# Optimization experiments

Measured on AMD Instinct MI355X. Metric: run time of the kernel, lower is better.

## Reference

```python
import jax, jax.numpy as jnp
import numpy as np

B, S, C, HEADS = 1, 4096, 640, 8
AH, AW = 64, 64            # attn-resolution grid, AH*AW == S
MH, MW = 512, 512          # full-res mask size
NEG = -1e9                 # finite large negative (safe for fully-masked rows)


def nearest_resize(x, h, w):
    # torch F.interpolate(mode='nearest'): idx = floor(i * H_in / H_out)
    H, W = x.shape[-2], x.shape[-1]
    ri = (jnp.arange(h) * H) // h
    ci = (jnp.arange(w) * W) // w
    return x[..., ri, :][..., :, ci]


def sdpa(q, k, v, mask, heads):
    # q,k,v: [B,S,C]; mask: [B,1,S,S] bool (True = attend), broadcasts over heads
    b, s, c = q.shape
    d = c // heads
    qh = q.reshape(b, s, heads, d).transpose(0, 2, 1, 3)  # bhsd
    kh = k.reshape(b, s, heads, d).transpose(0, 2, 1, 3)
    vh = v.reshape(b, s, heads, d).transpose(0, 2, 1, 3)
    scores = jnp.einsum('bhqd,bhkd->bhqk', qh, kh) / jnp.sqrt(jnp.asarray(d, qh.dtype))
    scores = jnp.where(mask, scores, NEG)
    attn = jax.nn.softmax(scores, axis=-1)
    out = jnp.einsum('bhqk,bhkd->bhqd', attn, vh)
    return out.transpose(0, 2, 1, 3).reshape(b, s, c)


def setup_inputs():
    key = jax.random.key(0)
    ks = jax.random.split(key, 14)
    std = 1.0 / np.sqrt(C)
    w = lambda k: (jax.random.normal(k, (C, C), jnp.float32) * std)
    return {
        'hidden_states': jax.random.normal(ks[0], (B, S, C), jnp.float32),
        'mask': jax.random.randint(ks[1], (B, 1, MH, MW), 0, 4, jnp.int32),
        'inpainting_mask': jax.random.randint(ks[2], (B, 1, MH, MW), 0, 2, jnp.int32),
        'Wq': w(ks[3]), 'Wk': w(ks[4]), 'Wv': w(ks[5]),
        'Wq_ent': w(ks[6]), 'Wk_ent': w(ks[7]), 'Wv_ent': w(ks[8]),
        'Wq_out': w(ks[9]), 'Wk_out': w(ks[10]), 'Wv_out': w(ks[11]),
        'Wo': w(ks[12]),
    }


def reference(hidden_states, mask, inpainting_mask, Wq, Wk, Wv,
              Wq_ent, Wk_ent, Wv_ent, Wq_out, Wk_out, Wv_out, Wo):
    residual = hidden_states
    b, s, c = hidden_states.shape

    # --- interpolation-derived masks (kept as [B,1,S,S]; broadcasts over heads) ---
    m = nearest_resize(mask, AH, AW).reshape(b, 1, s)                 # entity labels
    attn_mask = m[:, :, :, None] == m[:, :, None, :]                  # same-entity [B,1,S,S]
    im = nearest_resize(inpainting_mask, AH, AW).reshape(b, 1, s)
    outside_key = (im[:, :, None, :] == 0)                            # [B,1,1,S]
    attn_mask_outside = attn_mask & outside_key                       # [B,1,S,S]

    # --- projections ---
    q = hidden_states @ Wq.T
    k = hidden_states @ Wk.T
    v = hidden_states @ Wv.T
    q_e = hidden_states @ Wq_ent.T
    k_e = hidden_states @ Wk_ent.T
    v_e = hidden_states @ Wv_ent.T
    q_o = hidden_states @ Wq_out.T
    k_o = hidden_states @ Wk_out.T
    v_o = hidden_states @ Wv_out.T

    # --- three SDPA branches ---
    hs_orig = sdpa(q, k, v, attn_mask, HEADS)            # original attention
    hs_ent = sdpa(q_e, k_e, v_e, attn_mask, 1)           # entity attention (1 head)
    hs_out = sdpa(q_o, k_o, v_o, attn_mask_outside, HEADS)  # outside attention

    hs = hs_orig + hs_ent + hs_out
    return hs @ Wo.T + residual
```

## Files before the change

### kernel.cpp

```cpp
#include <hip/hip_runtime.h>
#include <cstdint>

typedef __attribute__((ext_vector_type(8))) short bf16x8;
typedef __attribute__((ext_vector_type(4))) short bf16x4;
typedef __attribute__((ext_vector_type(4))) float f32x4;

#define S_LEN 4096
#define CDIM  640
#define NPROJ 5760

__device__ __forceinline__ f32x4 mfma16(bf16x4 a, bf16x4 b, f32x4 c){
#if defined(__HIP_DEVICE_COMPILE__) && __HIP_DEVICE_COMPILE__
  return __builtin_amdgcn_mfma_f32_16x16x16bf16_1k(a, b, c, 0, 0, 0);
#else
  (void)a; (void)b;
  return c;
#endif
}

__device__ __forceinline__ void gload_lds(const unsigned short* g, unsigned short* l){
#if defined(__HIP_DEVICE_COMPILE__) && __HIP_DEVICE_COMPILE__
  __builtin_amdgcn_global_load_lds((const __attribute__((address_space(1))) unsigned int*)g,
                                   (__attribute__((address_space(3))) unsigned int*)l, 16, 0, 0);
#else
  (void)g; (void)l;
#endif
}

__device__ __forceinline__ unsigned short f2bf(float f){
  union { float f; uint32_t u; } v; v.f = f;
  uint32_t u = v.u;
  return (unsigned short)((u + 0x7fffu + ((u >> 16) & 1u)) >> 16);
}
__device__ __forceinline__ float b2f(unsigned short h){
  union { uint32_t u; float f; } v; v.u = ((uint32_t)h) << 16;
  return v.f;
}

__global__ void k_labels(const int* __restrict__ mask, const int* __restrict__ inp,
                         int* __restrict__ labels){
  int s = blockIdx.x * 256 + threadIdx.x;
  if (s >= S_LEN) return;
  int y = s >> 6, x = s & 63;
  int off = (y * 8) * 512 + x * 8;
  int m = mask[off] & 0xff;
  int o = (inp[off] == 0) ? 0x100 : 0;
  labels[s] = m | o;
}

__global__ void k_hist(const int* __restrict__ labels, int* __restrict__ boff, int* __restrict__ cnt){
  __shared__ int h[4];
  if (threadIdx.x < 4) h[threadIdx.x] = 0;
  __syncthreads();
  for (int s = threadIdx.x; s < S_LEN; s += 256) atomicAdd(&h[labels[s] & 3], 1);
  __syncthreads();
  if (threadIdx.x == 0){
    int a = 0;
    for (int c = 0; c < 4; c++){ boff[c] = a; a += h[c]; }
    boff[4] = a;
  }
  if (threadIdx.x < 4) cnt[threadIdx.x] = 0;
}

__global__ void k_perm(const int* __restrict__ labels, const int* __restrict__ boff,
                       int* __restrict__ cnt, int* __restrict__ perm,
                       int* __restrict__ inv, int* __restrict__ labP){
  int s = blockIdx.x * 256 + threadIdx.x;
  if (s >= S_LEN) return;
  int lab = labels[s];
  int c = lab & 3;
  int pos = boff[c] + atomicAdd(&cnt[c], 1);
  perm[pos] = s; inv[s] = pos; labP[pos] = lab;
}

__global__ void k_tiles(const int* __restrict__ labP, const int* __restrict__ boff,
                        int4* __restrict__ qtinfo, float* __restrict__ rowsum){
  int t = threadIdx.x;
  __shared__ int nkt[32];
  if (t < 32){
    int c0 = labP[t * 128] & 3, c1 = labP[t * 128 + 127] & 3;
    int lo = boff[c0] & ~127, hi = (boff[c1 + 1] + 127) & ~127;
    qtinfo[t].x = lo; qtinfo[t].y = hi; qtinfo[t].w = 0;
    nkt[t] = (hi - lo) >> 7;
  }
  __syncthreads();
  if (t == 0){
    int a = 0;
    for (int i = 0; i < 32; i++){ qtinfo[i].z = a; a += nkt[i]; }
  }
  for (int s = t; s < S_LEN; s += 256) rowsum[s] = 0.f;
}

__global__ void k_cvt_hs(const float* __restrict__ src, unsigned short* __restrict__ dst, int n){
  int idx = (blockIdx.x * 256 + threadIdx.x) * 4;
  if (idx >= n) return;
  float4 v = *(const float4*)(src + idx);
  ushort4 o;
  o.x = f2bf(v.x); o.y = f2bf(v.y); o.z = f2bf(v.z); o.w = f2bf(v.w);
  *(ushort4*)(dst + idx) = o;
}

struct WPtrs { const float* w[10]; };

__global__ void k_cvt_w(WPtrs p, unsigned short* __restrict__ dst){
  int e = (blockIdx.x * 256 + threadIdx.x) * 4;
  if (e >= 10 * 409600) return;
  int a = e / 409600, r = e % 409600;
  float sc = (a == 0 || a == 6) ? 0.11180339887498948f
           : (a == 3 ? 0.03952847075210474f : 1.0f);
  float4 v = *(const float4*)(p.w[a] + r);
  ushort4 o;
  o.x = f2bf(v.x * sc); o.y = f2bf(v.y * sc); o.z = f2bf(v.z * sc); o.w = f2bf(v.w * sc);
  *(ushort4*)(dst + e) = o;
}

template<int EPI>
__global__ __launch_bounds__(256) void k_gemm(const unsigned short* __restrict__ A,
                                              const unsigned short* __restrict__ B,
                                              int M, int N, int K, int ldc,
                                              const int* __restrict__ rowmap,
                                              unsigned short* __restrict__ Cb,
                                              float* __restrict__ Cf,
                                              const float* __restrict__ resid){
  __shared__ __align__(16) unsigned short As[128 * 64];
  __shared__ __align__(16) unsigned short Bs[128 * 64];
  int m0 = blockIdx.y * 128, n0 = blockIdx.x * 128;
  int tid = threadIdx.x;
  int wid = tid >> 6, lane = tid & 63;
  int quad = lane >> 4, l16 = lane & 15;
  int wm = (wid >> 1) * 64, wn = (wid & 1) * 64;
  f32x4 acc[4][4];
#pragma unroll
  for (int i = 0; i < 4; i++)
#pragma unroll
    for (int j = 0; j < 4; j++) acc[i][j] = f32x4{0.f, 0.f, 0.f, 0.f};

  for (int k0 = 0; k0 < K; k0 += 64){
    __syncthreads();
#pragma unroll
    for (int u = 0; u < 4; u++){
      int c = tid + u * 256;
      int row = c >> 3, off = (c & 7) * 8;
      gload_lds(&A[(size_t)(m0 + row) * K + k0 + off], &As[c * 8]);
      gload_lds(&B[(size_t)(n0 + row) * K + k0 + off], &Bs[c * 8]);
    }
    __syncthreads();
#pragma unroll
    for (int ks = 0; ks < 2; ks++){
      bf16x8 af[4], bfr[4];
#pragma unroll
      for (int t = 0; t < 4; t++){
        af[t]  = *(const bf16x8*)(&As[(wm + t * 16 + l16) * 64 + ks * 32 + quad * 8]);
        bfr[t] = *(const bf16x8*)(&Bs[(wn + t * 16 + l16) * 64 + ks * 32 + quad * 8]);
      }
#pragma unroll
      for (int mt = 0; mt < 4; mt++)
#pragma unroll
        for (int nt = 0; nt < 4; nt++)
          acc[mt][nt] = __builtin_amdgcn_mfma_f32_16x16x32_bf16(af[mt], bfr[nt], acc[mt][nt], 0, 0, 0);
    }
  }
#pragma unroll
  for (int mt = 0; mt < 4; mt++)
#pragma unroll
    for (int nt = 0; nt < 4; nt++)
#pragma unroll
      for (int r = 0; r < 4; r++){
        int row = m0 + wm + mt * 16 + quad * 4 + r;
        int col = n0 + wn + nt * 16 + l16;
        float v = acc[mt][nt][r];
        if (EPI == 0){
          Cb[(size_t)rowmap[row] * ldc + col] = f2bf(v);
        } else {
          int ro = rowmap[row];
          Cf[(size_t)ro * ldc + col] = v + resid[(size_t)ro * ldc + col];
        }
      }
}

__global__ void k_transpose_v(const unsigned short* __restrict__ proj, unsigned short* __restrict__ vT){
  __shared__ unsigned short T[64][65];
  int z = blockIdx.z;
  int s0 = blockIdx.x * 64, c0 = blockIdx.y * 64;
  int colbase = 1280 + z * 1920 + c0;
  unsigned short* dst = vT + (size_t)z * CDIM * S_LEN;
  int tid = threadIdx.x;
  for (int i = tid; i < 64 * 64; i += 256){
    int r = i >> 6, c = i & 63;
    T[r][c] = proj[(size_t)(s0 + r) * NPROJ + colbase + c];
  }
  __syncthreads();
  for (int i = tid; i < 64 * 64; i += 256){
    int c = i >> 6, r = i & 63;
    dst[(size_t)(c0 + c) * S_LEN + s0 + r] = T[r][c];
  }
}

#define KP 84
#define VP 76
__global__ __launch_bounds__(512, 2) void k_attn80(const unsigned short* __restrict__ proj,
                                                   const unsigned short* __restrict__ vT,
                                                   const int* __restrict__ labP,
                                                   const int4* __restrict__ qtinfo,
                                                   unsigned short* __restrict__ opart,
                                                   float* __restrict__ lpP){
  __shared__ __align__(16) unsigned short Ks[2][64 * KP];
  __shared__ __align__(16) unsigned short Vt[2][80 * VP];
  __shared__ __align__(16) int labk[2][64];
  int tid = threadIdx.x, wid = tid >> 6, lane = tid & 63;
  int quad = lane >> 4, l16 = lane & 15;
  int qt = blockIdx.x >> 1, half = blockIdx.x & 1;
  int q0 = qt * 256;
  int h  = blockIdx.y;
  bool OUTSIDE = (blockIdx.z == 1);
  int qc = (OUTSIDE ? 3840 : 0) + h * 80;
  int kc = (OUTSIDE ? 4480 : 640) + h * 80;
  const unsigned short* vTb = vT + (size_t)(OUTSIDE ? 2 : 0) * CDIM * S_LEN;
  int4 qa = qtinfo[qt * 2], qb = qtinfo[qt * 2 + 1];
  int lo = min(qa.x, qb.x), hi = max(qa.y, qb.y);
  int t0 = lo >> 6, t1 = hi >> 6;
  int nt = t1 - t0;
  int mid = t0 + ((nt + 1) >> 1);
  int ta = half ? mid : t0;
  int tb = half ? t1 : mid;

  int qrow0 = q0 + wid * 32 + l16;
  int qrow1 = qrow0 + 16;
  bf16x4 qf0[5], qf1[5];
#pragma unroll
  for (int dc = 0; dc < 5; dc++){
    qf0[dc] = *(const bf16x4*)&proj[(size_t)qrow0 * NPROJ + qc + dc * 16 + quad * 4];
    qf1[dc] = *(const bf16x4*)&proj[(size_t)qrow1 * NPROJ + qc + dc * 16 + quad * 4];
  }
  int lq0 = labP[qrow0] & 0xff, lq1 = labP[qrow1] & 0xff;

  float lp0 = 0.f, lp1 = 0.f;
  f32x4 Oc0[5], Oc1[5];
#pragma unroll
  for (int t = 0; t < 5; t++){ Oc0[t] = f32x4{0.f,0.f,0.f,0.f}; Oc1[t] = f32x4{0.f,0.f,0.f,0.f}; }

  const bool ISK = (tid < 256);
  const int t5 = ISK ? tid : (tid - 256);
  const unsigned short* gb = ISK ? proj : vTb;
  const int km = ISK ? NPROJ : 1;
  int ga0, ga1, ga2, ga3, ga4, ls0, ls1, ls2, ls3, ls4;
  {
    const int c0_ = t5, c1_ = t5 + 256, c2_ = t5 + 512, c3_ = t5 + 768, c4_ = t5 + 1024;
    if (ISK){
      ga0 = (c0_ / 20) * NPROJ + kc + (c0_ % 20) * 4;
      ga1 = (c1_ / 20) * NPROJ + kc + (c1_ % 20) * 4;
      ga2 = (c2_ / 20) * NPROJ + kc + (c2_ % 20) * 4;
      ga3 = (c3_ / 20) * NPROJ + kc + (c3_ % 20) * 4;
      ga4 = (c4_ / 20) * NPROJ + kc + (c4_ % 20) * 4;
      ls0 = (c0_ / 20) * KP + (c0_ % 20) * 4;
      ls1 = (c1_ / 20) * KP + (c1_ % 20) * 4;
      ls2 = (c2_ / 20) * KP + (c2_ % 20) * 4;
      ls3 = (c3_ / 20) * KP + (c3_ % 20) * 4;
      ls4 = (c4_ / 20) * KP + (c4_ % 20) * 4;
    } else {
      ga0 = (h * 80 + (c0_ >> 4)) * S_LEN + (c0_ & 15) * 4;
      ga1 = (h * 80 + (c1_ >> 4)) * S_LEN + (c1_ & 15) * 4;
      ga2 = (h * 80 + (c2_ >> 4)) * S_LEN + (c2_ & 15) * 4;
      ga3 = (h * 80 + (c3_ >> 4)) * S_LEN + (c3_ & 15) * 4;
      ga4 = (h * 80 + (c4_ >> 4)) * S_LEN + (c4_ & 15) * 4;
      ls0 = (c0_ >> 4) * VP + (c0_ & 15) * 4;
      ls1 = (c1_ >> 4) * VP + (c1_ & 15) * 4;
      ls2 = (c2_ >> 4) * VP + (c2_ & 15) * 4;
      ls3 = (c3_ >> 4) * VP + (c3_ & 15) * 4;
      ls4 = (c4_ >> 4) * VP + (c4_ & 15) * 4;
    }
  }

  uint2 r0, r1, r2, r3, r4;
  int lreg = 0;

#define LOADT(kt_) do {                                              \
    size_t _ob = (size_t)((kt_) * 64) * (size_t)km;                  \
    r0 = *(const uint2*)&gb[_ob + ga0];                              \
    r1 = *(const uint2*)&gb[_ob + ga1];                              \
    r2 = *(const uint2*)&gb[_ob + ga2];                              \
    r3 = *(const uint2*)&gb[_ob + ga3];                              \
    r4 = *(const uint2*)&gb[_ob + ga4];                              \
    if (tid < 64) lreg = labP[(kt_) * 64 + tid];                     \
  } while (0)

#define WRITET(b) do {                                               \
    unsigned short* _lb = ISK ? Ks[b] : Vt[b];                       \
    *(uint2*)&_lb[ls0] = r0;                                         \
    *(uint2*)&_lb[ls1] = r1;                                         \
    *(uint2*)&_lb[ls2] = r2;                                         \
    *(uint2*)&_lb[ls3] = r3;                                         \
    *(uint2*)&_lb[ls4] = r4;                                         \
    if (tid < 64) labk[b][tid] = lreg;                               \
  } while (0)

  LOADT(ta);
  WRITET(0);
  if (ta + 1 < tb) LOADT(ta + 1);
  __syncthreads();

  int cur = 0;
  for (int kt = ta; kt < tb; kt++){
    int nxt = cur ^ 1;
    if (kt + 1 < tb){
      WRITET(nxt);
      if (kt + 2 < tb) LOADT(kt + 2);
    }

#pragma unroll
    for (int kg = 0; kg < 4; kg++){
      f32x4 sa0 = f32x4{0.f,0.f,0.f,0.f}, sa1 = f32x4{0.f,0.f,0.f,0.f};
#pragma unroll
      for (int dc = 0; dc < 5; dc++){
        bf16x4 kf = *(const bf16x4*)&Ks[cur][(kg * 16 + l16) * KP + dc * 16 + quad * 4];
        sa0 = mfma16(kf, qf0[dc], sa0);
        sa1 = mfma16(kf, qf1[dc], sa1);
      }
      int4 lk4 = *(const int4*)&labk[cur][kg * 16 + quad * 4];
      bool m0 = !OUTSIDE || (lk4.x & 0x100), m1 = !OUTSIDE || (lk4.y & 0x100);
      bool m2 = !OUTSIDE || (lk4.z & 0x100), m3 = !OUTSIDE || (lk4.w & 0x100);
      int k0l = lk4.x & 0xff, k1l = lk4.y & 0xff, k2l = lk4.z & 0xff, k3l = lk4.w & 0xff;
      bf16x4 pf0, pf1;
      {
        float p0 = (k0l == lq0 && m0) ? __expf(sa0[0]) : 0.f;
        float p1 = (k1l == lq0 && m1) ? __expf(sa0[1]) : 0.f;
        float p2 = (k2l == lq0 && m2) ? __expf(sa0[2]) : 0.f;
        float p3 = (k3l == lq0 && m3) ? __expf(sa0[3]) : 0.f;
        lp0 += (p0 + p1) + (p2 + p3);
        pf0[0] = (short)f2bf(p0); pf0[1] = (short)f2bf(p1);
        pf0[2] = (short)f2bf(p2); pf0[3] = (short)f2bf(p3);
      }
      {
        float p0 = (k0l == lq1 && m0) ? __expf(sa1[0]) : 0.f;
        float p1 = (k1l == lq1 && m1) ? __expf(sa1[1]) : 0.f;
        float p2 = (k2l == lq1 && m2) ? __expf(sa1[2]) : 0.f;
        float p3 = (k3l == lq1 && m3) ? __expf(sa1[3]) : 0.f;
        lp1 += (p0 + p1) + (p2 + p3);
        pf1[0] = (short)f2bf(p0); pf1[1] = (short)f2bf(p1);
        pf1[2] = (short)f2bf(p2); pf1[3] = (short)f2bf(p3);
      }
#pragma unroll
      for (int dt = 0; dt < 5; dt++){
        bf16x4 vf = *(const bf16x4*)&Vt[cur][(dt * 16 + l16) * VP + kg * 16 + quad * 4];
        Oc0[dt] = mfma16(vf, pf0, Oc0[dt]);
        Oc1[dt] = mfma16(vf, pf1, Oc1[dt]);
      }
    }
    __syncthreads();
    cur = nxt;
  }
#undef LOADT
#undef WRITET
  lp0 += __shfl_xor(lp0, 16); lp0 += __shfl_xor(lp0, 32);
  lp1 += __shfl_xor(lp1, 16); lp1 += __shfl_xor(lp1, 32);
  int hz = half * 2 + (int)blockIdx.z;
  if (quad == 0){
    lpP[(size_t)(hz * 8 + h) * S_LEN + qrow0] = lp0;
    lpP[(size_t)(hz * 8 + h) * S_LEN + qrow1] = lp1;
  }
  unsigned short* dst = opart + (size_t)hz * S_LEN * CDIM;
#pragma unroll
  for (int dt = 0; dt < 5; dt++){
    ushort4 o;
    o.x = f2bf(Oc0[dt][0]); o.y = f2bf(Oc0[dt][1]);
    o.z = f2bf(Oc0[dt][2]); o.w = f2bf(Oc0[dt][3]);
    *(ushort4*)&dst[(size_t)qrow0 * CDIM + h * 80 + dt * 16 + quad * 4] = o;
    o.x = f2bf(Oc1[dt][0]); o.y = f2bf(Oc1[dt][1]);
    o.z = f2bf(Oc1[dt][2]); o.w = f2bf(Oc1[dt][3]);
    *(ushort4*)&dst[(size_t)qrow1 * CDIM + h * 80 + dt * 16 + quad * 4] = o;
  }
}

__global__ __launch_bounds__(256) void k_comb(const unsigned short* __restrict__ opart,
                                              const float* __restrict__ lpP,
                                              unsigned short* __restrict__ planes){
  int i = blockIdx.x * 256 + threadIdx.x;
  int z = blockIdx.y;
  int qrow = i / 160, c4 = (i % 160) * 4;
  int h = c4 / 80;
  size_t o0 = ((size_t)(z)     * S_LEN + qrow) * CDIM + c4;
  size_t o1 = ((size_t)(2 + z) * S_LEN + qrow) * CDIM + c4;
  float lp = lpP[(size_t)(z * 8 + h) * S_LEN + qrow]
           + lpP[(size_t)((2 + z) * 8 + h) * S_LEN + qrow];
  float iL = 1.f / lp;
  ushort4 a = *(const ushort4*)&opart[o0];
  ushort4 b = *(const ushort4*)&opart[o1];
  ushort4 o;
  o.x = f2bf((b2f(a.x) + b2f(b.x)) * iL);
  o.y = f2bf((b2f(a.y) + b2f(b.y)) * iL);
  o.z = f2bf((b2f(a.z) + b2f(b.z)) * iL);
  o.w = f2bf((b2f(a.w) + b2f(b.w)) * iL);
  *(ushort4*)&planes[(size_t)z * S_LEN * CDIM + (size_t)qrow * CDIM + c4] = o;
}

__global__ __launch_bounds__(256) void k_ent_qk(const unsigned short* __restrict__ proj,
                                                const int* __restrict__ labP,
                                                const int4* __restrict__ qtinfo,
                                                unsigned short* __restrict__ Sbuf,
                                                float* __restrict__ rowsum){
  int qt = blockIdx.y;
  int4 qi = qtinfo[qt];
  int nkt = (qi.y - qi.x) >> 7;
  if ((int)blockIdx.x >= nkt) return;
  int m0 = qt * 128, n0 = qi.x + blockIdx.x * 128;
  __shared__ __align__(16) unsigned short As[128 * 64];
  __shared__ __align__(16) unsigned short Bs[128 * 64];
  __shared__ int lQ[128], lK[128];
  int tid = threadIdx.x, wid = tid >> 6, lane = tid & 63;
  int quad = lane >> 4, l16 = lane & 15;
  int wm = (wid >> 1) * 64, wn = (wid & 1) * 64;
  if (tid < 128) lQ[tid] = labP[m0 + tid] & 0xff;
  else           lK[tid - 128] = labP[n0 + tid - 128] & 0xff;
  f32x4 acc[4][4];
#pragma unroll
  for (int i = 0; i < 4; i++)
#pragma unroll
    for (int j = 0; j < 4; j++) acc[i][j] = f32x4{0.f, 0.f, 0.f, 0.f};

  for (int k0 = 0; k0 < 640; k0 += 64){
    __syncthreads();
#pragma unroll
    for (int u = 0; u < 4; u++){
      int c = tid + u * 256;
      int row = c >> 3, off = (c & 7) * 8;
      gload_lds(&proj[(size_t)(m0 + row) * NPROJ + 1920 + k0 + off], &As[c * 8]);
      gload_lds(&proj[(size_t)(n0 + row) * NPROJ + 2560 + k0 + off], &Bs[c * 8]);
    }
    __syncthreads();
#pragma unroll
    for (int ks = 0; ks < 2; ks++){
      bf16x8 af[4], bfr[4];
#pragma unroll
      for (int t = 0; t < 4; t++){
        af[t]  = *(const bf16x8*)(&As[(wm + t * 16 + l16) * 64 + ks * 32 + quad * 8]);
        bfr[t] = *(const bf16x8*)(&Bs[(wn + t * 16 + l16) * 64 + ks * 32 + quad * 8]);
      }
#pragma unroll
      for (int mt = 0; mt < 4; mt++)
#pragma unroll
        for (int nt = 0; nt < 4; nt++)
          acc[mt][nt] = __builtin_amdgcn_mfma_f32_16x16x32_bf16(af[mt], bfr[nt], acc[mt][nt], 0, 0, 0);
    }
  }
  unsigned short* St = Sbuf + ((size_t)(qi.z + blockIdx.x)) * 16384;
#pragma unroll
  for (int mt = 0; mt < 4; mt++)
#pragma unroll
    for (int r = 0; r < 4; r++){
      int lrow = wm + mt * 16 + quad * 4 + r;
      int myq = lQ[lrow];
      float psum = 0.f;
#pragma unroll
      for (int nt = 0; nt < 4; nt++){
        int lcol = wn + nt * 16 + l16;
        float p = (myq == lK[lcol]) ? __expf(acc[mt][nt][r]) : 0.f;
        St[lrow * 128 + lcol] = f2bf(p);
        psum += p;
      }
#pragma unroll
      for (int m = 1; m < 16; m <<= 1) psum += __shfl_xor(psum, m);
      if (l16 == 0) atomicAdd(&rowsum[m0 + lrow], psum);
    }
}

__global__ __launch_bounds__(256) void k_ent_pv(const unsigned short* __restrict__ Sbuf,
                                                const unsigned short* __restrict__ veT,
                                                const int4* __restrict__ qtinfo,
                                                const float* __restrict__ rowsum,
                                                const unsigned short* __restrict__ planes,
                                                unsigned short* __restrict__ attnS){
  int qt = blockIdx.y, d0 = blockIdx.x * 128;
  int4 qi = qtinfo[qt];
  int m0 = qt * 128;
  int nk = qi.y - qi.x;
  __shared__ __align__(16) unsigned short As[128 * 32];
  __shared__ __align__(16) unsigned short Bs[128 * 32];
  int tid = threadIdx.x, wid = tid >> 6, lane = tid & 63;
  int quad = lane >> 4, l16 = lane & 15;
  int wm = (wid >> 1) * 64, wn = (wid & 1) * 64;
  f32x4 acc[4][4];
#pragma unroll
  for (int i = 0; i < 4; i++)
#pragma unroll
    for (int j = 0; j < 4; j++) acc[i][j] = f32x4{0.f, 0.f, 0.f, 0.f};

  for (int kk = 0; kk < nk; kk += 32){
    const unsigned short* St = Sbuf + ((size_t)(qi.z + (kk >> 7))) * 16384;
    int kloc = kk & 127;
    __syncthreads();
#pragma unroll
    for (int u = 0; u < 2; u++){
      int c = tid + u * 256;
      int row = c >> 2, off = (c & 3) * 8;
      gload_lds(&St[row * 128 + kloc + off], &As[c * 8]);
      gload_lds(&veT[(size_t)(d0 + row) * S_LEN + qi.x + kk + off], &Bs[c * 8]);
    }
    __syncthreads();
    bf16x8 af[4], bfr[4];
#pragma unroll
    for (int t = 0; t < 4; t++){
      af[t]  = *(const bf16x8*)(&As[(wm + t * 16 + l16) * 32 + quad * 8]);
      bfr[t] = *(const bf16x8*)(&Bs[(wn + t * 16 + l16) * 32 + quad * 8]);
    }
#pragma unroll
    for (int mt = 0; mt < 4; mt++)
#pragma unroll
      for (int nt = 0; nt < 4; nt++)
        acc[mt][nt] = __builtin_amdgcn_mfma_f32_16x16x32_bf16(af[mt], bfr[nt], acc[mt][nt], 0, 0, 0);
  }
#pragma unroll
  for (int mt = 0; mt < 4; mt++)
#pragma unroll
    for (int r = 0; r < 4; r++){
      int row = m0 + wm + mt * 16 + quad * 4 + r;
      float invL = 1.f / rowsum[row];
#pragma unroll
      for (int nt = 0; nt < 4; nt++){
        int col = d0 + wn + nt * 16 + l16;
        size_t idx = (size_t)row * CDIM + col;
        float v = acc[mt][nt][r] * invL + b2f(planes[idx]) + b2f(planes[(size_t)S_LEN * CDIM + idx]);
        attnS[idx] = f2bf(v);
      }
    }
}

extern "C" void kernel_launch(void* const* d_in, const int* in_sizes, int n_in,
                              void* d_out, int out_size, void* d_ws, size_t ws_size,
                              hipStream_t stream){
  const float* hs  = (const float*)d_in[0];
  const int* mask  = (const int*)d_in[1];
  const int* inp   = (const int*)d_in[2];
  char* ws = (char*)d_ws;
  int*            labels  = (int*)(ws + 0);
  int*            boff    = (int*)(ws + 16384);
  int*            cnt     = (int*)(ws + 16640);
  int*            perm    = (int*)(ws + 16896);
  int*            inv     = (int*)(ws + 33280);
  int*            labP    = (int*)(ws + 49664);
  int4*           qtinfo  = (int4*)(ws + 66560);
  float*          rowsum  = (float*)(ws + 67072);
  unsigned short* hsb     = (unsigned short*)(ws + 131072);
  unsigned short* Wall    = (unsigned short*)(ws + 5373952);
  unsigned short* proj    = (unsigned short*)(ws + 13565952);
  unsigned short* vT      = (unsigned short*)(ws + 60751872);
  unsigned short* planes  = (unsigned short*)(ws + 76480512);
  unsigned short* Sbuf    = (unsigned short*)(ws + 86966272);
  unsigned short* attnS   = (unsigned short*)(ws + 120520704);
  unsigned short* Wob     = Wall + 9 * 409600;
  unsigned short* opart   = Sbuf;
  float*          lpP     = (float*)(ws + 86966272 + 20971520);

  k_labels<<<16, 256, 0, stream>>>(mask, inp, labels);
  k_hist<<<1, 256, 0, stream>>>(labels, boff, cnt);
  k_perm<<<16, 256, 0, stream>>>(labels, boff, cnt, perm, inv, labP);
  k_tiles<<<1, 256, 0, stream>>>(labP, boff, qtinfo, rowsum);
  k_cvt_hs<<<(S_LEN * CDIM / 4 + 255) / 256, 256, 0, stream>>>(hs, hsb, S_LEN * CDIM);
  WPtrs wp;
  for (int i = 0; i < 10; i++) wp.w[i] = (const float*)d_in[3 + i];
  k_cvt_w<<<(10 * 409600 / 4 + 255) / 256, 256, 0, stream>>>(wp, Wall);

  k_gemm<0><<<dim3(45, 32), 256, 0, stream>>>(hsb, Wall, S_LEN, NPROJ, CDIM, NPROJ,
                                              inv, proj, nullptr, nullptr);
  k_transpose_v<<<dim3(64, 10, 3), 256, 0, stream>>>(proj, vT);

  k_attn80<<<dim3(32, 8, 2), 512, 0, stream>>>(proj, vT, labP, qtinfo, opart, lpP);
  k_comb<<<dim3(2560, 2), 256, 0, stream>>>(opart, lpP, planes);

  k_ent_qk<<<dim3(32, 32), 256, 0, stream>>>(proj, labP, qtinfo, Sbuf, rowsum);
  k_ent_pv<<<dim3(5, 32), 256, 0, stream>>>(Sbuf, vT + (size_t)1 * CDIM * S_LEN,
                                            qtinfo, rowsum, planes, attnS);

  k_gemm<1><<<dim3(5, 32), 256, 0, stream>>>(attnS, Wob, S_LEN, CDIM, CDIM, CDIM,
                                             perm, nullptr, (float*)d_out, hs);
}
```

Measured before the change: 404.3 us.

## Split attention key range three ways and deepen entity PV k-step

The masked attention kernel now splits each query tile's key range into three parts instead of two, launching 48 instead of 32 blocks along x. The combine kernel sums three partial outputs and row sums, and the lpP buffer moves to make room for the third partial plane. This aims to raise occupancy across the GPU's compute units, at the cost of extra partial-result traffic and combine work. Separately, the entity PV GEMM loads 64-wide K slices per barrier pair instead of 32, halving sync overhead but doubling LDS use.

```diff
diff --git a/kernel.cpp b/kernel.cpp
--- a/kernel.cpp
+++ b/kernel.cpp
@@ -209,7 +209,7 @@
   __shared__ __align__(16) int labk[2][64];
   int tid = threadIdx.x, wid = tid >> 6, lane = tid & 63;
   int quad = lane >> 4, l16 = lane & 15;
-  int qt = blockIdx.x >> 1, half = blockIdx.x & 1;
+  int qt = blockIdx.x / 3, third = blockIdx.x % 3;
   int q0 = qt * 256;
   int h  = blockIdx.y;
   bool OUTSIDE = (blockIdx.z == 1);
@@ -220,9 +220,8 @@
   int lo = min(qa.x, qb.x), hi = max(qa.y, qb.y);
   int t0 = lo >> 6, t1 = hi >> 6;
   int nt = t1 - t0;
-  int mid = t0 + ((nt + 1) >> 1);
-  int ta = half ? mid : t0;
-  int tb = half ? t1 : mid;
+  int ta = t0 + (nt * third) / 3;
+  int tb = t0 + (nt * (third + 1)) / 3;
 
   int qrow0 = q0 + wid * 32 + l16;
   int qrow1 = qrow0 + 16;
@@ -294,66 +293,68 @@
     if (tid < 64) labk[b][tid] = lreg;                               \
   } while (0)
 
-  LOADT(ta);
-  WRITET(0);
-  if (ta + 1 < tb) LOADT(ta + 1);
-  __syncthreads();
-
-  int cur = 0;
-  for (int kt = ta; kt < tb; kt++){
-    int nxt = cur ^ 1;
-    if (kt + 1 < tb){
-      WRITET(nxt);
-      if (kt + 2 < tb) LOADT(kt + 2);
-    }
-
-#pragma unroll
-    for (int kg = 0; kg < 4; kg++){
-      f32x4 sa0 = f32x4{0.f,0.f,0.f,0.f}, sa1 = f32x4{0.f,0.f,0.f,0.f};
-#pragma unroll
-      for (int dc = 0; dc < 5; dc++){
-        bf16x4 kf = *(const bf16x4*)&Ks[cur][(kg * 16 + l16) * KP + dc * 16 + quad * 4];
-        sa0 = mfma16(kf, qf0[dc], sa0);
-        sa1 = mfma16(kf, qf1[dc], sa1);
-      }
-      int4 lk4 = *(const int4*)&labk[cur][kg * 16 + quad * 4];
-      bool m0 = !OUTSIDE || (lk4.x & 0x100), m1 = !OUTSIDE || (lk4.y & 0x100);
-      bool m2 = !OUTSIDE || (lk4.z & 0x100), m3 = !OUTSIDE || (lk4.w & 0x100);
-      int k0l = lk4.x & 0xff, k1l = lk4.y & 0xff, k2l = lk4.z & 0xff, k3l = lk4.w & 0xff;
-      bf16x4 pf0, pf1;
-      {
-        float p0 = (k0l == lq0 && m0) ? __expf(sa0[0]) : 0.f;
-        float p1 = (k1l == lq0 && m1) ? __expf(sa0[1]) : 0.f;
-        float p2 = (k2l == lq0 && m2) ? __expf(sa0[2]) : 0.f;
-        float p3 = (k3l == lq0 && m3) ? __expf(sa0[3]) : 0.f;
-        lp0 += (p0 + p1) + (p2 + p3);
-        pf0[0] = (short)f2bf(p0); pf0[1] = (short)f2bf(p1);
-        pf0[2] = (short)f2bf(p2); pf0[3] = (short)f2bf(p3);
-      }
-      {
-        float p0 = (k0l == lq1 && m0) ? __expf(sa1[0]) : 0.f;
-        float p1 = (k1l == lq1 && m1) ? __expf(sa1[1]) : 0.f;
-        float p2 = (k2l == lq1 && m2) ? __expf(sa1[2]) : 0.f;
-        float p3 = (k3l == lq1 && m3) ? __expf(sa1[3]) : 0.f;
-        lp1 += (p0 + p1) + (p2 + p3);
-        pf1[0] = (short)f2bf(p0); pf1[1] = (short)f2bf(p1);
-        pf1[2] = (short)f2bf(p2); pf1[3] = (short)f2bf(p3);
-      }
-#pragma unroll
-      for (int dt = 0; dt < 5; dt++){
-        bf16x4 vf = *(const bf16x4*)&Vt[cur][(dt * 16 + l16) * VP + kg * 16 + quad * 4];
-        Oc0[dt] = mfma16(vf, pf0, Oc0[dt]);
-        Oc1[dt] = mfma16(vf, pf1, Oc1[dt]);
-      }
-    }
-    __syncthreads();
-    cur = nxt;
+  if (ta < tb){
+    LOADT(ta);
+    WRITET(0);
+    if (ta + 1 < tb) LOADT(ta + 1);
+    __syncthreads();
+
+    int cur = 0;
+    for (int kt = ta; kt < tb; kt++){
+      int nxt = cur ^ 1;
+      if (kt + 1 < tb){
+        WRITET(nxt);
+        if (kt + 2 < tb) LOADT(kt + 2);
+      }
+
+#pragma unroll
+      for (int kg = 0; kg < 4; kg++){
+        f32x4 sa0 = f32x4{0.f,0.f,0.f,0.f}, sa1 = f32x4{0.f,0.f,0.f,0.f};
+#pragma unroll
+        for (int dc = 0; dc < 5; dc++){
+          bf16x4 kf = *(const bf16x4*)&Ks[cur][(kg * 16 + l16) * KP + dc * 16 + quad * 4];
+          sa0 = mfma16(kf, qf0[dc], sa0);
+          sa1 = mfma16(kf, qf1[dc], sa1);
+        }
+        int4 lk4 = *(const int4*)&labk[cur][kg * 16 + quad * 4];
+        bool m0 = !OUTSIDE || (lk4.x & 0x100), m1 = !OUTSIDE || (lk4.y & 0x100);
+        bool m2 = !OUTSIDE || (lk4.z & 0x100), m3 = !OUTSIDE || (lk4.w & 0x100);
+        int k0l = lk4.x & 0xff, k1l = lk4.y & 0xff, k2l = lk4.z & 0xff, k3l = lk4.w & 0xff;
+        bf16x4 pf0, pf1;
+        {
+          float p0 = (k0l == lq0 && m0) ? __expf(sa0[0]) : 0.f;
+          float p1 = (k1l == lq0 && m1) ? __expf(sa0[1]) : 0.f;
+          float p2 = (k2l == lq0 && m2) ? __expf(sa0[2]) : 0.f;
+          float p3 = (k3l == lq0 && m3) ? __expf(sa0[3]) : 0.f;
+          lp0 += (p0 + p1) + (p2 + p3);
+          pf0[0] = (short)f2bf(p0); pf0[1] = (short)f2bf(p1);
+          pf0[2] = (short)f2bf(p2); pf0[3] = (short)f2bf(p3);
+        }
+        {
+          float p0 = (k0l == lq1 && m0) ? __expf(sa1[0]) : 0.f;
+          float p1 = (k1l == lq1 && m1) ? __expf(sa1[1]) : 0.f;
+          float p2 = (k2l == lq1 && m2) ? __expf(sa1[2]) : 0.f;
+          float p3 = (k3l == lq1 && m3) ? __expf(sa1[3]) : 0.f;
+          lp1 += (p0 + p1) + (p2 + p3);
+          pf1[0] = (short)f2bf(p0); pf1[1] = (short)f2bf(p1);
+          pf1[2] = (short)f2bf(p2); pf1[3] = (short)f2bf(p3);
+        }
+#pragma unroll
+        for (int dt = 0; dt < 5; dt++){
+          bf16x4 vf = *(const bf16x4*)&Vt[cur][(dt * 16 + l16) * VP + kg * 16 + quad * 4];
+          Oc0[dt] = mfma16(vf, pf0, Oc0[dt]);
+          Oc1[dt] = mfma16(vf, pf1, Oc1[dt]);
+        }
+      }
+      __syncthreads();
+      cur = nxt;
+    }
   }
 #undef LOADT
 #undef WRITET
   lp0 += __shfl_xor(lp0, 16); lp0 += __shfl_xor(lp0, 32);
   lp1 += __shfl_xor(lp1, 16); lp1 += __shfl_xor(lp1, 32);
-  int hz = half * 2 + (int)blockIdx.z;
+  int hz = third * 2 + (int)blockIdx.z;
   if (quad == 0){
     lpP[(size_t)(hz * 8 + h) * S_LEN + qrow0] = lp0;
     lpP[(size_t)(hz * 8 + h) * S_LEN + qrow1] = lp1;
@@ -378,19 +379,21 @@
   int z = blockIdx.y;
   int qrow = i / 160, c4 = (i % 160) * 4;
   int h = c4 / 80;
-  size_t o0 = ((size_t)(z)     * S_LEN + qrow) * CDIM + c4;
-  size_t o1 = ((size_t)(2 + z) * S_LEN + qrow) * CDIM + c4;
-  float lp = lpP[(size_t)(z * 8 + h) * S_LEN + qrow]
-           + lpP[(size_t)((2 + z) * 8 + h) * S_LEN + qrow];
+  size_t base = (size_t)qrow * CDIM + c4;
+  size_t pz = (size_t)S_LEN * CDIM;
+  float lp = lpP[(size_t)((z)     * 8 + h) * S_LEN + qrow]
+           + lpP[(size_t)((z + 2) * 8 + h) * S_LEN + qrow]
+           + lpP[(size_t)((z + 4) * 8 + h) * S_LEN + qrow];
   float iL = 1.f / lp;
-  ushort4 a = *(const ushort4*)&opart[o0];
-  ushort4 b = *(const ushort4*)&opart[o1];
+  ushort4 a = *(const ushort4*)&opart[(size_t)(z)     * pz + base];
+  ushort4 b = *(const ushort4*)&opart[(size_t)(z + 2) * pz + base];
+  ushort4 c = *(const ushort4*)&opart[(size_t)(z + 4) * pz + base];
   ushort4 o;
-  o.x = f2bf((b2f(a.x) + b2f(b.x)) * iL);
-  o.y = f2bf((b2f(a.y) + b2f(b.y)) * iL);
-  o.z = f2bf((b2f(a.z) + b2f(b.z)) * iL);
-  o.w = f2bf((b2f(a.w) + b2f(b.w)) * iL);
-  *(ushort4*)&planes[(size_t)z * S_LEN * CDIM + (size_t)qrow * CDIM + c4] = o;
+  o.x = f2bf((b2f(a.x) + b2f(b.x) + b2f(c.x)) * iL);
+  o.y = f2bf((b2f(a.y) + b2f(b.y) + b2f(c.y)) * iL);
+  o.z = f2bf((b2f(a.z) + b2f(b.z) + b2f(c.z)) * iL);
+  o.w = f2bf((b2f(a.w) + b2f(b.w) + b2f(c.w)) * iL);
+  *(ushort4*)&planes[(size_t)z * pz + base] = o;
 }
 
 __global__ __launch_bounds__(256) void k_ent_qk(const unsigned short* __restrict__ proj,
@@ -473,8 +476,8 @@
   int4 qi = qtinfo[qt];
   int m0 = qt * 128;
   int nk = qi.y - qi.x;
-  __shared__ __align__(16) unsigned short As[128 * 32];
-  __shared__ __align__(16) unsigned short Bs[128 * 32];
+  __shared__ __align__(16) unsigned short As[128 * 64];
+  __shared__ __align__(16) unsigned short Bs[128 * 64];
   int tid = threadIdx.x, wid = tid >> 6, lane = tid & 63;
   int quad = lane >> 4, l16 = lane & 15;
   int wm = (wid >> 1) * 64, wn = (wid & 1) * 64;
@@ -484,29 +487,32 @@
 #pragma unroll
     for (int j = 0; j < 4; j++) acc[i][j] = f32x4{0.f, 0.f, 0.f, 0.f};
 
-  for (int kk = 0; kk < nk; kk += 32){
+  for (int kk = 0; kk < nk; kk += 64){
     const unsigned short* St = Sbuf + ((size_t)(qi.z + (kk >> 7))) * 16384;
     int kloc = kk & 127;
     __syncthreads();
 #pragma unroll
-    for (int u = 0; u < 2; u++){
+    for (int u = 0; u < 4; u++){
       int c = tid + u * 256;
-      int row = c >> 2, off = (c & 3) * 8;
+      int row = c >> 3, off = (c & 7) * 8;
       gload_lds(&St[row * 128 + kloc + off], &As[c * 8]);
       gload_lds(&veT[(size_t)(d0 + row) * S_LEN + qi.x + kk + off], &Bs[c * 8]);
     }
     __syncthreads();
-    bf16x8 af[4], bfr[4];
-#pragma unroll
-    for (int t = 0; t < 4; t++){
-      af[t]  = *(const bf16x8*)(&As[(wm + t * 16 + l16) * 32 + quad * 8]);
-      bfr[t] = *(const bf16x8*)(&Bs[(wn + t * 16 + l16) * 32 + quad * 8]);
-    }
-#pragma unroll
-    for (int mt = 0; mt < 4; mt++)
-#pragma unroll
-      for (int nt = 0; nt < 4; nt++)
-        acc[mt][nt] = __builtin_amdgcn_mfma_f32_16x16x32_bf16(af[mt], bfr[nt], acc[mt][nt], 0, 0, 0);
+#pragma unroll
+    for (int ks = 0; ks < 2; ks++){
+      bf16x8 af[4], bfr[4];
+#pragma unroll
+      for (int t = 0; t < 4; t++){
+        af[t]  = *(const bf16x8*)(&As[(wm + t * 16 + l16) * 64 + ks * 32 + quad * 8]);
+        bfr[t] = *(const bf16x8*)(&Bs[(wn + t * 16 + l16) * 64 + ks * 32 + quad * 8]);
+      }
+#pragma unroll
+      for (int mt = 0; mt < 4; mt++)
+#pragma unroll
+        for (int nt = 0; nt < 4; nt++)
+          acc[mt][nt] = __builtin_amdgcn_mfma_f32_16x16x32_bf16(af[mt], bfr[nt], acc[mt][nt], 0, 0, 0);
+    }
   }
 #pragma unroll
   for (int mt = 0; mt < 4; mt++)
@@ -548,7 +554,7 @@
   unsigned short* attnS   = (unsigned short*)(ws + 120520704);
   unsigned short* Wob     = Wall + 9 * 409600;
   unsigned short* opart   = Sbuf;
-  float*          lpP     = (float*)(ws + 86966272 + 20971520);
+  float*          lpP     = (float*)(ws + 86966272 + 31457280);
 
   k_labels<<<16, 256, 0, stream>>>(mask, inp, labels);
   k_hist<<<1, 256, 0, stream>>>(labels, boff, cnt);
@@ -563,7 +569,7 @@
                                               inv, proj, nullptr, nullptr);
   k_transpose_v<<<dim3(64, 10, 3), 256, 0, stream>>>(proj, vT);
 
-  k_attn80<<<dim3(32, 8, 2), 512, 0, stream>>>(proj, vT, labP, qtinfo, opart, lpP);
+  k_attn80<<<dim3(48, 8, 2), 512, 0, stream>>>(proj, vT, labP, qtinfo, opart, lpP);
   k_comb<<<dim3(2560, 2), 256, 0, stream>>>(opart, lpP, planes);
 
   k_ent_qk<<<dim3(32, 32), 256, 0, stream>>>(proj, labP, qtinfo, Sbuf, rowsum);
```

New measurement: 402.2 us. About the same (-0.5%).
